# Kernel tuning notes

Measured on AMD Instinct MI355X. Metric: run time of the kernel, lower is better.

Reference implementation:

```python
import jax, jax.numpy as jnp
import numpy as np


def setup_inputs() -> dict:
    key = jax.random.key(0)
    k1, k2 = jax.random.split(key)
    embeddings = jax.random.normal(k1, (32, 512, 1024), dtype=jnp.float32)
    aspect = jax.random.normal(k2, (32, 1024), dtype=jnp.float32)
    return {"embeddings": embeddings, "aspect": aspect}


def reference(embeddings, aspect):
    # go_backwards=False, so no sequence reversal.
    # L2-normalize embeddings per token and aspect per sample.
    e = embeddings / jnp.linalg.norm(embeddings, axis=2, keepdims=True)
    a = aspect / jnp.linalg.norm(aspect, axis=1, keepdims=True)
    # NaN-mask (zero-norm rows produce NaN after division).
    e = jnp.where(jnp.isnan(e), jnp.zeros_like(e), e)
    a = jnp.where(jnp.isnan(a), jnp.zeros_like(a), a)
    # Circulant matrix: circ[b, i, j] = a[b, (j - i) mod D]
    # (matches the TF scatter_nd construction M[i, (i+k)%D] = a[k]).
    D = e.shape[-1]
    r = jnp.arange(D)
    idx = (r[None, :] - r[:, None]) % D  # [D, D]
    circ = a[:, idx]  # [B, D, D]
    # matmul(e, circ, transpose_b=True): out[b,s,i] = sum_j e[b,s,j] * circ[b,i,j]
    return jnp.einsum('bsd,bid->bsi', e, circ)
```

## Files before the change

kernel.cpp:

```cpp
#include <hip/hip_runtime.h>
#include <hip/hip_bf16.h>

typedef __attribute__((ext_vector_type(8))) short bf16x8;
typedef __attribute__((ext_vector_type(4))) float f32x4;

#define NB 32
#define NS 512
#define ND 1024

__device__ __forceinline__ unsigned short f2bf(float f) {
  unsigned int u = __float_as_uint(f);
  u = (u + 0x7FFFu + ((u >> 16) & 1u)) >> 16;
  return (unsigned short)u;
}

__global__ void anorm_kernel(const float* __restrict__ aspect,
                             unsigned short* __restrict__ a_n) {
  int b = blockIdx.x;
  int t = threadIdx.x;
  const float4* p = (const float4*)(aspect + (size_t)b * ND);
  float4 v = p[t];
  float s = v.x * v.x + v.y * v.y + v.z * v.z + v.w * v.w;
#pragma unroll
  for (int off = 32; off >= 1; off >>= 1) s += __shfl_down(s, off);
  __shared__ float red[4];
  if ((t & 63) == 0) red[t >> 6] = s;
  __syncthreads();
  float tot = red[0] + red[1] + red[2] + red[3];
  float inv = (tot > 0.f) ? (1.f / sqrtf(tot)) : 0.f;
  ushort4 u;
  u.x = f2bf(v.x * inv); u.y = f2bf(v.y * inv);
  u.z = f2bf(v.z * inv); u.w = f2bf(v.w * inv);
  ((ushort4*)(a_n + (size_t)b * ND))[t] = u;
}

__global__ __launch_bounds__(256)
void enormbf_kernel(const float* __restrict__ emb,
                    unsigned short* __restrict__ eN) {
  int wave = threadIdx.x >> 6, lane = threadIdx.x & 63;
  size_t row = (size_t)blockIdx.x * 4 + wave;
  const float4* p = (const float4*)(emb + row * ND);
  float4 v[4];
  float s = 0.f;
#pragma unroll
  for (int j = 0; j < 4; ++j) {
    v[j] = p[lane + 64 * j];
    s += v[j].x * v[j].x + v[j].y * v[j].y + v[j].z * v[j].z + v[j].w * v[j].w;
  }
#pragma unroll
  for (int off = 32; off >= 1; off >>= 1) s += __shfl_xor(s, off);
  float inv = (s > 0.f) ? (1.f / sqrtf(s)) : 0.f;
  ushort4* o = (ushort4*)(eN + row * ND);
#pragma unroll
  for (int j = 0; j < 4; ++j) {
    ushort4 u;
    u.x = f2bf(v[j].x * inv); u.y = f2bf(v[j].y * inv);
    u.z = f2bf(v[j].z * inv); u.w = f2bf(v[j].w * inv);
    o[lane + 64 * j] = u;
  }
}

__global__ __launch_bounds__(512, 2)
void corr_gemm4_kernel(const unsigned short* __restrict__ eN,
                       const unsigned short* __restrict__ a_n,
                       float* __restrict__ out) {
  __shared__ __align__(16) unsigned short Alds[3 * 16384];
  __shared__ __align__(16) unsigned short copies[8 * 1288];

  const int b = blockIdx.x, mt = blockIdx.y, nt = blockIdx.z;
  const int n0 = nt * 256, m0 = mt * 256;
  const int tid = threadIdx.x;

  {
    const unsigned short* an = a_n + (size_t)b * ND;
    const int p = tid & 7;
    const int x0 = (tid >> 3) * 20;
    const int base = (768 - n0 + p) & 1023;
#pragma unroll
    for (int j = 0; j < 20; j += 4) {
      ushort4 u;
      u.x = an[(base + x0 + j + 0) & 1023];
      u.y = an[(base + x0 + j + 1) & 1023];
      u.z = an[(base + x0 + j + 2) & 1023];
      u.w = an[(base + x0 + j + 3) & 1023];
      *(ushort4*)&copies[p * 1288 + x0 + j] = u;
    }
  }

  const int lane = tid & 63, wv = tid >> 6;
  const int wm = wv >> 2, wn = wv & 3;
  const int q = lane >> 4, l16 = lane & 15;
  const int mx = l16 & 7;
  const int s00 = (q ^ mx) * 8;
  const int s01 = ((4 + q) ^ mx) * 8;
  const int arow = (wm * 128 + l16) * 64;

  const int pB = (8 - mx) & 7;
  const unsigned short* Bp = copies + pB * 1287 + (256 + 8 * q - wn * 64 - l16);

  const unsigned short* gstage =
      eN + ((size_t)b * NS + m0 + (tid >> 3)) * ND + (size_t)(((tid & 7) ^ ((tid >> 3) & 7)) * 8);
  char* ldsAbase = (char*)Alds;

  f32x4 acc[8][4];
#pragma unroll
  for (int i = 0; i < 8; ++i)
#pragma unroll
    for (int j = 0; j < 4; ++j)
      acc[i][j] = (f32x4){0.f, 0.f, 0.f, 0.f};

  __syncthreads();
#pragma unroll
  for (int j = 0; j < 4; ++j)
    __builtin_amdgcn_global_load_lds(
        (const __attribute__((address_space(1))) void*)(gstage + (size_t)j * 64 * ND),
        (__attribute__((address_space(3))) void*)(ldsAbase + (size_t)tid * 16 + j * 8192),
        16, 0, 0);
#pragma unroll
  for (int j = 0; j < 4; ++j)
    __builtin_amdgcn_global_load_lds(
        (const __attribute__((address_space(1))) void*)(gstage + (size_t)j * 64 * ND + 64),
        (__attribute__((address_space(3))) void*)(ldsAbase + 32768 + (size_t)tid * 16 + j * 8192),
        16, 0, 0);
  asm volatile("s_waitcnt vmcnt(4)" ::: "memory");
  __builtin_amdgcn_sched_barrier(0);
  __builtin_amdgcn_s_barrier();

  int c0 = 0, c1 = 1, c2 = 2;

#define STAGE_PAIR(J0)                                                                   \
  do {                                                                                   \
    if (kt + 2 < 16) {                                                                   \
      const unsigned short* sg_ = gstage + (size_t)(kt + 2) * 64;                        \
      char* dl_ = ldsAbase + c2 * 32768 + (size_t)tid * 16;                              \
      __builtin_amdgcn_global_load_lds(                                                  \
          (const __attribute__((address_space(1))) void*)(sg_ + (size_t)(J0) * 64 * ND), \
          (__attribute__((address_space(3))) void*)(dl_ + (J0) * 8192), 16, 0, 0);       \
      __builtin_amdgcn_global_load_lds(                                                  \
          (const __attribute__((address_space(1))) void*)(sg_ + (size_t)((J0) + 1) * 64 * ND), \
          (__attribute__((address_space(3))) void*)(dl_ + ((J0) + 1) * 8192), 16, 0, 0); \
    }                                                                                    \
  } while (0)

#define GEMM_PHASE(PH, EXTRA)                                                            \
  do {                                                                                   \
    bf16x8 aA0  = *(const bf16x8*)&At[arow + (PH)*2048 + s00];                           \
    bf16x8 aA0k = *(const bf16x8*)&At[arow + (PH)*2048 + s01];                           \
    bf16x8 aA1  = *(const bf16x8*)&At[arow + (PH)*2048 + 1024 + s00];                    \
    bf16x8 aA1k = *(const bf16x8*)&At[arow + (PH)*2048 + 1024 + s01];                    \
    EXTRA;                                                                               \
    __builtin_amdgcn_s_barrier();                                                        \
    asm volatile("s_waitcnt lgkmcnt(0)" ::: "memory");                                   \
    __builtin_amdgcn_sched_barrier(0);                                                   \
    __builtin_amdgcn_s_setprio(1);                                                       \
    _Pragma("unroll")                                                                    \
    for (int n = 0; n < 4; ++n) {                                                        \
      acc[2*(PH)][n]   = __builtin_amdgcn_mfma_f32_16x16x32_bf16(aA0,  bfr[n][0], acc[2*(PH)][n],   0, 0, 0); \
      acc[2*(PH)][n]   = __builtin_amdgcn_mfma_f32_16x16x32_bf16(aA0k, bfr[n][1], acc[2*(PH)][n],   0, 0, 0); \
      acc[2*(PH)+1][n] = __builtin_amdgcn_mfma_f32_16x16x32_bf16(aA1,  bfr[n][0], acc[2*(PH)+1][n], 0, 0, 0); \
      acc[2*(PH)+1][n] = __builtin_amdgcn_mfma_f32_16x16x32_bf16(aA1k, bfr[n][1], acc[2*(PH)+1][n], 0, 0, 0); \
    }                                                                                    \
    __builtin_amdgcn_s_setprio(0);                                                       \
  } while (0)

#pragma unroll 1
  for (int kt = 0; kt < 16; ++kt) {
    const unsigned short* At = Alds + c0 * 16384;

    bf16x8 bfr[4][2];
    {
      const unsigned short* Bt = Bp + kt * 64;
#pragma unroll
      for (int n = 0; n < 4; ++n) {
        bfr[n][0] = *(const bf16x8*)(Bt - n * 16);
        bfr[n][1] = *(const bf16x8*)(Bt + 32 - n * 16);
      }
    }
    GEMM_PHASE(0, STAGE_PAIR(0));
    __builtin_amdgcn_s_barrier();
    GEMM_PHASE(1, STAGE_PAIR(2));
    __builtin_amdgcn_s_barrier();
    GEMM_PHASE(2, );
    __builtin_amdgcn_s_barrier();
    GEMM_PHASE(3, );
    if (kt < 14) {
      asm volatile("s_waitcnt vmcnt(4)" ::: "memory");
    } else if (kt == 14) {
      asm volatile("s_waitcnt vmcnt(0)" ::: "memory");
    }
    __builtin_amdgcn_sched_barrier(0);
    __builtin_amdgcn_s_barrier();

    int tmp = c0; c0 = c1; c1 = c2; c2 = tmp;
  }
#undef GEMM_PHASE
#undef STAGE_PAIR

  float* outB = out + ((size_t)b * NS + m0) * ND + n0;
#pragma unroll
  for (int i = 0; i < 8; ++i) {
#pragma unroll
    for (int rg = 0; rg < 4; ++rg) {
      int r = wm * 128 + i * 16 + q * 4 + rg;
      float* orow = outB + (size_t)r * ND + wn * 64 + l16;
#pragma unroll
      for (int n = 0; n < 4; ++n)
        orow[n * 16] = acc[i][n][rg];
    }
  }
}

__global__ void enorm_kernel(const float* __restrict__ emb,
                             float* __restrict__ inv_norm) {
  int wave = threadIdx.x >> 6;
  int lane = threadIdx.x & 63;
  int row = blockIdx.x * 4 + wave;
  const float4* p = (const float4*)(emb + (size_t)row * ND);
  float s = 0.f;
#pragma unroll
  for (int j = 0; j < 4; ++j) {
    float4 v = p[lane + 64 * j];
    s += v.x * v.x + v.y * v.y + v.z * v.z + v.w * v.w;
  }
#pragma unroll
  for (int off = 32; off >= 1; off >>= 1) s += __shfl_down(s, off);
  if (lane == 0) inv_norm[row] = (s > 0.f) ? (1.f / sqrtf(s)) : 0.f;
}

__global__ __launch_bounds__(256)
void corr_gemm_kernel(const float* __restrict__ emb,
                      const float* __restrict__ inv_norm,
                      const unsigned short* __restrict__ a_n,
                      float* __restrict__ out) {
  __shared__ unsigned short copies[8][2056];
  __shared__ unsigned short Atile[128][40];

  const int nt = blockIdx.x, mt = blockIdx.y, b = blockIdx.z;
  const int n0 = nt * 128, m0 = mt * 128;
  const int t = threadIdx.x;

  {
    const unsigned short* an = a_n + (size_t)b * ND;
    int p = t & 7;
    int x0 = (t >> 3) * 64;
#pragma unroll
    for (int j = 0; j < 64; j += 4) {
      ushort4 u;
      u.x = an[(x0 + j + 0 + p) & 1023];
      u.y = an[(x0 + j + 1 + p) & 1023];
      u.z = an[(x0 + j + 2 + p) & 1023];
      u.w = an[(x0 + j + 3 + p) & 1023];
      *(ushort4*)&copies[p][x0 + j] = u;
    }
  }

  const int ar = t >> 3;
  const int ac = (t & 7) * 4;
  float invn[4];
#pragma unroll
  for (int w = 0; w < 4; ++w)
    invn[w] = inv_norm[b * NS + m0 + ar + 32 * w];

  const int lane = t & 63;
  const int wv = t >> 6;
  const int wm = wv >> 1, wn = wv & 1;
  const int q = lane >> 4, l16 = lane & 15;

  f32x4 acc[4][4];
#pragma unroll
  for (int i = 0; i < 4; ++i)
#pragma unroll
    for (int j = 0; j < 4; ++j)
      acc[i][j] = (f32x4){0.f, 0.f, 0.f, 0.f};

  const float* embB = emb + ((size_t)b * NS + m0) * ND;

  for (int k0 = 0; k0 < ND; k0 += 32) {
    __syncthreads();
#pragma unroll
    for (int w = 0; w < 4; ++w) {
      int r = ar + 32 * w;
      float4 v = *(const float4*)(embB + (size_t)r * ND + k0 + ac);
      float in = invn[w];
      ushort4 u;
      u.x = f2bf(v.x * in); u.y = f2bf(v.y * in);
      u.z = f2bf(v.z * in); u.w = f2bf(v.w * in);
      *(ushort4*)&Atile[r][ac] = u;
    }
    __syncthreads();

    bf16x8 af[4], bfr[4];
#pragma unroll
    for (int r = 0; r < 4; ++r) {
      int m = wm * 64 + r * 16 + l16;
      af[r] = *(const bf16x8*)&Atile[m][q * 8];
    }
#pragma unroll
    for (int r = 0; r < 4; ++r) {
      int ng = n0 + wn * 64 + r * 16 + l16;
      int e0 = k0 + 8 * q - ng + 1024;
      int p = e0 & 7;
      bfr[r] = *(const bf16x8*)&copies[p][e0 - p];
    }
#pragma unroll
    for (int i = 0; i < 4; ++i)
#pragma unroll
      for (int j = 0; j < 4; ++j)
        acc[i][j] = __builtin_amdgcn_mfma_f32_16x16x32_bf16(af[i], bfr[j], acc[i][j], 0, 0, 0);
  }

  float* outB = out + ((size_t)b * NS + m0) * ND + n0;
#pragma unroll
  for (int i = 0; i < 4; ++i) {
#pragma unroll
    for (int rg = 0; rg < 4; ++rg) {
      int s = wm * 64 + i * 16 + q * 4 + rg;
      float* orow = outB + (size_t)s * ND + wn * 64 + l16;
#pragma unroll
      for (int j = 0; j < 4; ++j)
        orow[j * 16] = acc[i][j][rg];
    }
  }
}

extern "C" void kernel_launch(void* const* d_in, const int* in_sizes, int n_in,
                              void* d_out, int out_size, void* d_ws, size_t ws_size,
                              hipStream_t stream) {
  const float* emb = (const float*)d_in[0];
  const float* aspect = (const float*)d_in[1];
  float* out = (float*)d_out;

  const size_t need = 65536 + (size_t)NB * NS * ND * 2;

  if (ws_size >= need) {
    unsigned short* a_n = (unsigned short*)d_ws;
    unsigned short* eN = (unsigned short*)((char*)d_ws + 65536);
    anorm_kernel<<<NB, 256, 0, stream>>>(aspect, a_n);
    enormbf_kernel<<<4096, 256, 0, stream>>>(emb, eN);
    corr_gemm4_kernel<<<dim3(NB, 2, 4), 512, 0, stream>>>(eN, a_n, out);
  } else {
    float* inv_norm = (float*)d_ws;
    unsigned short* a_n = (unsigned short*)((char*)d_ws + 65536);
    enorm_kernel<<<4096, 256, 0, stream>>>(emb, inv_norm);
    anorm_kernel<<<NB, 256, 0, stream>>>(aspect, a_n);
    corr_gemm_kernel<<<dim3(8, 4, NB), 256, 0, stream>>>(emb, inv_norm, a_n, out);
  }
}
```

Baseline: 144.4 us.

## Fuse aspect normalization into embedding kernel and software-pipeline LDS A-fragment loads

```diff
diff --git a/kernel.cpp b/kernel.cpp
--- a/kernel.cpp
+++ b/kernel.cpp
@@ -14,29 +14,11 @@
   return (unsigned short)u;
 }
 
-__global__ void anorm_kernel(const float* __restrict__ aspect,
-                             unsigned short* __restrict__ a_n) {
-  int b = blockIdx.x;
-  int t = threadIdx.x;
-  const float4* p = (const float4*)(aspect + (size_t)b * ND);
-  float4 v = p[t];
-  float s = v.x * v.x + v.y * v.y + v.z * v.z + v.w * v.w;
-#pragma unroll
-  for (int off = 32; off >= 1; off >>= 1) s += __shfl_down(s, off);
-  __shared__ float red[4];
-  if ((t & 63) == 0) red[t >> 6] = s;
-  __syncthreads();
-  float tot = red[0] + red[1] + red[2] + red[3];
-  float inv = (tot > 0.f) ? (1.f / sqrtf(tot)) : 0.f;
-  ushort4 u;
-  u.x = f2bf(v.x * inv); u.y = f2bf(v.y * inv);
-  u.z = f2bf(v.z * inv); u.w = f2bf(v.w * inv);
-  ((ushort4*)(a_n + (size_t)b * ND))[t] = u;
-}
-
 __global__ __launch_bounds__(256)
-void enormbf_kernel(const float* __restrict__ emb,
-                    unsigned short* __restrict__ eN) {
+void enormbf_fused_kernel(const float* __restrict__ emb,
+                          unsigned short* __restrict__ eN,
+                          const float* __restrict__ aspect,
+                          unsigned short* __restrict__ a_n) {
   int wave = threadIdx.x >> 6, lane = threadIdx.x & 63;
   size_t row = (size_t)blockIdx.x * 4 + wave;
   const float4* p = (const float4*)(emb + row * ND);
@@ -58,10 +40,29 @@
     u.z = f2bf(v[j].z * inv); u.w = f2bf(v[j].w * inv);
     o[lane + 64 * j] = u;
   }
+
+  if (blockIdx.x < NB) {
+    int b = blockIdx.x;
+    int t = threadIdx.x;
+    const float4* pa = (const float4*)(aspect + (size_t)b * ND);
+    float4 va = pa[t];
+    float sa = va.x * va.x + va.y * va.y + va.z * va.z + va.w * va.w;
+#pragma unroll
+    for (int off = 32; off >= 1; off >>= 1) sa += __shfl_down(sa, off);
+    __shared__ float red[4];
+    if ((t & 63) == 0) red[t >> 6] = sa;
+    __syncthreads();
+    float tot = red[0] + red[1] + red[2] + red[3];
+    float inva = (tot > 0.f) ? (1.f / sqrtf(tot)) : 0.f;
+    ushort4 u;
+    u.x = f2bf(va.x * inva); u.y = f2bf(va.y * inva);
+    u.z = f2bf(va.z * inva); u.w = f2bf(va.w * inva);
+    ((ushort4*)(a_n + (size_t)b * ND))[t] = u;
+  }
 }
 
 __global__ __launch_bounds__(512, 2)
-void corr_gemm4_kernel(const unsigned short* __restrict__ eN,
+void corr_gemm5_kernel(const unsigned short* __restrict__ eN,
                        const unsigned short* __restrict__ a_n,
                        float* __restrict__ out) {
   __shared__ __align__(16) unsigned short Alds[3 * 16384];
@@ -70,22 +71,6 @@
   const int b = blockIdx.x, mt = blockIdx.y, nt = blockIdx.z;
   const int n0 = nt * 256, m0 = mt * 256;
   const int tid = threadIdx.x;
-
-  {
-    const unsigned short* an = a_n + (size_t)b * ND;
-    const int p = tid & 7;
-    const int x0 = (tid >> 3) * 20;
-    const int base = (768 - n0 + p) & 1023;
-#pragma unroll
-    for (int j = 0; j < 20; j += 4) {
-      ushort4 u;
-      u.x = an[(base + x0 + j + 0) & 1023];
-      u.y = an[(base + x0 + j + 1) & 1023];
-      u.z = an[(base + x0 + j + 2) & 1023];
-      u.w = an[(base + x0 + j + 3) & 1023];
-      *(ushort4*)&copies[p * 1288 + x0 + j] = u;
-    }
-  }
 
   const int lane = tid & 63, wv = tid >> 6;
   const int wm = wv >> 2, wn = wv & 3;
@@ -102,14 +87,16 @@
       eN + ((size_t)b * NS + m0 + (tid >> 3)) * ND + (size_t)(((tid & 7) ^ ((tid >> 3) & 7)) * 8);
   char* ldsAbase = (char*)Alds;
 
-  f32x4 acc[8][4];
-#pragma unroll
-  for (int i = 0; i < 8; ++i)
-#pragma unroll
-    for (int j = 0; j < 4; ++j)
-      acc[i][j] = (f32x4){0.f, 0.f, 0.f, 0.f};
-
-  __syncthreads();
+  unsigned short av[20];
+  {
+    const unsigned short* an = a_n + (size_t)b * ND;
+    const int p = tid & 7;
+    const int x0 = (tid >> 3) * 20;
+    const int base = (768 - n0 + p) & 1023;
+#pragma unroll
+    for (int j = 0; j < 20; ++j) av[j] = an[(base + x0 + j) & 1023];
+  }
+
 #pragma unroll
   for (int j = 0; j < 4; ++j)
     __builtin_amdgcn_global_load_lds(
@@ -122,11 +109,35 @@
         (const __attribute__((address_space(1))) void*)(gstage + (size_t)j * 64 * ND + 64),
         (__attribute__((address_space(3))) void*)(ldsAbase + 32768 + (size_t)tid * 16 + j * 8192),
         16, 0, 0);
+
+  {
+    const int p = tid & 7;
+    const int x0 = (tid >> 3) * 20;
+#pragma unroll
+    for (int j = 0; j < 20; ++j) copies[p * 1288 + x0 + j] = av[j];
+  }
+
+  f32x4 acc[8][4];
+#pragma unroll
+  for (int i = 0; i < 8; ++i)
+#pragma unroll
+    for (int j = 0; j < 4; ++j)
+      acc[i][j] = (f32x4){0.f, 0.f, 0.f, 0.f};
+
+  asm volatile("s_waitcnt lgkmcnt(0)" ::: "memory");
+  __builtin_amdgcn_s_barrier();
   asm volatile("s_waitcnt vmcnt(4)" ::: "memory");
-  __builtin_amdgcn_sched_barrier(0);
   __builtin_amdgcn_s_barrier();
 
-  int c0 = 0, c1 = 1, c2 = 2;
+  bf16x8 a0[4], a1[4], bfr[4][2];
+
+#define ISSUE_A(DST, BASE, PHN)                                          \
+  do {                                                                   \
+    DST[0] = *(const bf16x8*)&(BASE)[arow + (PHN) * 2048 + s00];         \
+    DST[1] = *(const bf16x8*)&(BASE)[arow + (PHN) * 2048 + s01];         \
+    DST[2] = *(const bf16x8*)&(BASE)[arow + (PHN) * 2048 + 1024 + s00];  \
+    DST[3] = *(const bf16x8*)&(BASE)[arow + (PHN) * 2048 + 1024 + s01];  \
+  } while (0)
 
 #define STAGE_PAIR(J0)                                                                   \
   do {                                                                                   \
@@ -142,32 +153,28 @@
     }                                                                                    \
   } while (0)
 
-#define GEMM_PHASE(PH, EXTRA)                                                            \
-  do {                                                                                   \
-    bf16x8 aA0  = *(const bf16x8*)&At[arow + (PH)*2048 + s00];                           \
-    bf16x8 aA0k = *(const bf16x8*)&At[arow + (PH)*2048 + s01];                           \
-    bf16x8 aA1  = *(const bf16x8*)&At[arow + (PH)*2048 + 1024 + s00];                    \
-    bf16x8 aA1k = *(const bf16x8*)&At[arow + (PH)*2048 + 1024 + s01];                    \
-    EXTRA;                                                                               \
-    __builtin_amdgcn_s_barrier();                                                        \
-    asm volatile("s_waitcnt lgkmcnt(0)" ::: "memory");                                   \
-    __builtin_amdgcn_sched_barrier(0);                                                   \
-    __builtin_amdgcn_s_setprio(1);                                                       \
-    _Pragma("unroll")                                                                    \
-    for (int n = 0; n < 4; ++n) {                                                        \
-      acc[2*(PH)][n]   = __builtin_amdgcn_mfma_f32_16x16x32_bf16(aA0,  bfr[n][0], acc[2*(PH)][n],   0, 0, 0); \
-      acc[2*(PH)][n]   = __builtin_amdgcn_mfma_f32_16x16x32_bf16(aA0k, bfr[n][1], acc[2*(PH)][n],   0, 0, 0); \
-      acc[2*(PH)+1][n] = __builtin_amdgcn_mfma_f32_16x16x32_bf16(aA1,  bfr[n][0], acc[2*(PH)+1][n], 0, 0, 0); \
-      acc[2*(PH)+1][n] = __builtin_amdgcn_mfma_f32_16x16x32_bf16(aA1k, bfr[n][1], acc[2*(PH)+1][n], 0, 0, 0); \
-    }                                                                                    \
-    __builtin_amdgcn_s_setprio(0);                                                       \
+#define MFMA_PH(PH, CS)                                                                       \
+  do {                                                                                        \
+    __builtin_amdgcn_s_setprio(1);                                                            \
+    _Pragma("unroll")                                                                         \
+    for (int n = 0; n < 4; ++n) {                                                             \
+      acc[2*(PH)][n]   = __builtin_amdgcn_mfma_f32_16x16x32_bf16(CS[0], bfr[n][0], acc[2*(PH)][n],   0, 0, 0); \
+      acc[2*(PH)][n]   = __builtin_amdgcn_mfma_f32_16x16x32_bf16(CS[1], bfr[n][1], acc[2*(PH)][n],   0, 0, 0); \
+      acc[2*(PH)+1][n] = __builtin_amdgcn_mfma_f32_16x16x32_bf16(CS[2], bfr[n][0], acc[2*(PH)+1][n], 0, 0, 0); \
+      acc[2*(PH)+1][n] = __builtin_amdgcn_mfma_f32_16x16x32_bf16(CS[3], bfr[n][1], acc[2*(PH)+1][n], 0, 0, 0); \
+    }                                                                                         \
+    __builtin_amdgcn_s_setprio(0);                                                            \
   } while (0)
+
+  int c0 = 0, c1 = 1, c2 = 2;
+
+  ISSUE_A(a0, Alds, 0);
 
 #pragma unroll 1
   for (int kt = 0; kt < 16; ++kt) {
     const unsigned short* At = Alds + c0 * 16384;
-
-    bf16x8 bfr[4][2];
+    const unsigned short* An = Alds + c1 * 16384;
+
     {
       const unsigned short* Bt = Bp + kt * 64;
 #pragma unroll
@@ -176,25 +183,53 @@
         bfr[n][1] = *(const bf16x8*)(Bt + 32 - n * 16);
       }
     }
-    GEMM_PHASE(0, STAGE_PAIR(0));
+    __builtin_amdgcn_sched_barrier(0);
+    ISSUE_A(a1, At, 1);
+    STAGE_PAIR(0);
+    __builtin_amdgcn_sched_barrier(0);
     __builtin_amdgcn_s_barrier();
-    GEMM_PHASE(1, STAGE_PAIR(2));
-    __builtin_amdgcn_s_barrier();
-    GEMM_PHASE(2, );
-    __builtin_amdgcn_s_barrier();
-    GEMM_PHASE(3, );
+    asm volatile("s_waitcnt lgkmcnt(4)" ::: "memory");
+    __builtin_amdgcn_sched_barrier(0);
+    MFMA_PH(0, a0);
+
+    ISSUE_A(a0, At, 2);
+    STAGE_PAIR(2);
     if (kt < 14) {
       asm volatile("s_waitcnt vmcnt(4)" ::: "memory");
-    } else if (kt == 14) {
+    } else {
       asm volatile("s_waitcnt vmcnt(0)" ::: "memory");
     }
     __builtin_amdgcn_sched_barrier(0);
     __builtin_amdgcn_s_barrier();
+    asm volatile("s_waitcnt lgkmcnt(4)" ::: "memory");
+    __builtin_amdgcn_sched_barrier(0);
+    MFMA_PH(1, a1);
+
+    ISSUE_A(a1, At, 3);
+    __builtin_amdgcn_sched_barrier(0);
+    __builtin_amdgcn_s_barrier();
+    asm volatile("s_waitcnt lgkmcnt(4)" ::: "memory");
+    __builtin_amdgcn_sched_barrier(0);
+    MFMA_PH(2, a0);
+
+    if (kt < 15) {
+      ISSUE_A(a0, An, 0);
+      __builtin_amdgcn_sched_barrier(0);
+      __builtin_amdgcn_s_barrier();
+      asm volatile("s_waitcnt lgkmcnt(4)" ::: "memory");
+    } else {
+      __builtin_amdgcn_s_barrier();
+      asm volatile("s_waitcnt lgkmcnt(0)" ::: "memory");
+    }
+    __builtin_amdgcn_sched_barrier(0);
+    MFMA_PH(3, a1);
+    __builtin_amdgcn_s_barrier();
 
     int tmp = c0; c0 = c1; c1 = c2; c2 = tmp;
   }
-#undef GEMM_PHASE
+#undef MFMA_PH
 #undef STAGE_PAIR
+#undef ISSUE_A
 
   float* outB = out + ((size_t)b * NS + m0) * ND + n0;
 #pragma unroll
@@ -208,6 +243,26 @@
         orow[n * 16] = acc[i][n][rg];
     }
   }
+}
+
+__global__ void anorm_kernel(const float* __restrict__ aspect,
+                             unsigned short* __restrict__ a_n) {
+  int b = blockIdx.x;
+  int t = threadIdx.x;
+  const float4* p = (const float4*)(aspect + (size_t)b * ND);
+  float4 v = p[t];
+  float s = v.x * v.x + v.y * v.y + v.z * v.z + v.w * v.w;
+#pragma unroll
+  for (int off = 32; off >= 1; off >>= 1) s += __shfl_down(s, off);
+  __shared__ float red[4];
+  if ((t & 63) == 0) red[t >> 6] = s;
+  __syncthreads();
+  float tot = red[0] + red[1] + red[2] + red[3];
+  float inv = (tot > 0.f) ? (1.f / sqrtf(tot)) : 0.f;
+  ushort4 u;
+  u.x = f2bf(v.x * inv); u.y = f2bf(v.y * inv);
+  u.z = f2bf(v.z * inv); u.w = f2bf(v.w * inv);
+  ((ushort4*)(a_n + (size_t)b * ND))[t] = u;
 }
 
 __global__ void enorm_kernel(const float* __restrict__ emb,
@@ -335,9 +390,8 @@
   if (ws_size >= need) {
     unsigned short* a_n = (unsigned short*)d_ws;
     unsigned short* eN = (unsigned short*)((char*)d_ws + 65536);
-    anorm_kernel<<<NB, 256, 0, stream>>>(aspect, a_n);
-    enormbf_kernel<<<4096, 256, 0, stream>>>(emb, eN);
-    corr_gemm4_kernel<<<dim3(NB, 2, 4), 512, 0, stream>>>(eN, a_n, out);
+    enormbf_fused_kernel<<<4096, 256, 0, stream>>>(emb, eN, aspect, a_n);
+    corr_gemm5_kernel<<<dim3(NB, 2, 4), 512, 0, stream>>>(eN, a_n, out);
   } else {
     float* inv_norm = (float*)d_ws;
     unsigned short* a_n = (unsigned short*)((char*)d_ws + 65536);
```

Result: faster. 141.0 us (-2.4%).
